# Kernel tuning notes

Hardware: AMD Instinct MI355X
Metric: run time of the kernel (lower is better)

The kernel has to match this reference:

```python
import jax, jax.numpy as jnp
import numpy as np

HID = 1024
HEADS = 16
HEAD_DIM = HID // HEADS
INTER = 4 * HID
EPS = 1e-6
SCALE = 1.0 / np.sqrt(HEAD_DIM)


def setup_inputs() -> dict:
    key = jax.random.key(0)
    ks = jax.random.split(key, 8)
    s = 0.02
    return {
        "x": jax.random.normal(ks[0], (2, 2048, HID), dtype=jnp.float32),
        "wq": jax.random.normal(ks[1], (HID, HID), dtype=jnp.float32) * s,
        "wk": jax.random.normal(ks[2], (HID, HID), dtype=jnp.float32) * s,
        "wv": jax.random.normal(ks[3], (HID, HID), dtype=jnp.float32) * s,
        "wo": jax.random.normal(ks[4], (HID, HID), dtype=jnp.float32) * s,
        "w_gate": jax.random.normal(ks[5], (INTER, HID), dtype=jnp.float32) * s,
        "w_up": jax.random.normal(ks[6], (INTER, HID), dtype=jnp.float32) * s,
        "w_down": jax.random.normal(ks[7], (HID, INTER), dtype=jnp.float32) * s,
        "norm1_w": jnp.ones((HID,), dtype=jnp.float32),
        "norm2_w": jnp.ones((HID,), dtype=jnp.float32),
    }


def _rmsnorm(x, w):
    rms = jnp.sqrt(jnp.mean(x * x, axis=-1, keepdims=True) + EPS)
    return x / rms * w


def reference(x, wq, wk, wv, wo, w_gate, w_up, w_down, norm1_w, norm2_w):
    b, s, _ = x.shape
    residual = x
    h = _rmsnorm(x, norm1_w)
    # projections: nn.Linear computes h @ W.T
    q = (h @ wq.T).reshape(b, s, HEADS, HEAD_DIM).transpose(0, 2, 1, 3)
    k = (h @ wk.T).reshape(b, s, HEADS, HEAD_DIM).transpose(0, 2, 1, 3)
    v = (h @ wv.T).reshape(b, s, HEADS, HEAD_DIM).transpose(0, 2, 1, 3)
    scores = jnp.einsum("bhqd,bhkd->bhqk", q, k) * SCALE
    attn = jax.nn.softmax(scores, axis=-1)
    out = jnp.einsum("bhqk,bhkd->bhqd", attn, v)
    out = out.transpose(0, 2, 1, 3).reshape(b, s, HID)
    x = residual + out @ wo.T
    residual = x
    h = _rmsnorm(x, norm2_w)
    gate = jax.nn.silu(h @ w_gate.T)
    up = h @ w_up.T
    mlp_out = (gate * up) @ w_down.T
    return residual + mlp_out
```

## Files before the change

### kernel.cpp

```cpp
#include <hip/hip_runtime.h>
#include <hip/hip_bf16.h>

#define HID 1024
#define SEQ 2048
#define NTOK 4096
#define ATT_SCALE 0.125f

typedef __attribute__((ext_vector_type(4))) float f32x4;
typedef __attribute__((ext_vector_type(16))) float f32x16;
typedef __attribute__((ext_vector_type(8))) __bf16 bf16x8;
typedef __attribute__((ext_vector_type(4))) __bf16 bf16x4;
typedef __bf16 bf16;

__device__ __forceinline__ bf16 f2bf(float f) { return (bf16)f; }

__device__ __forceinline__ void gld_lds16(const void* g, void* l) {
  __builtin_amdgcn_global_load_lds((const __attribute__((address_space(1))) void*)g,
                                   (__attribute__((address_space(3))) void*)l,
                                   16, 0, 0);
}

__device__ __forceinline__ f32x4 mfma16(bf16x8 a, bf16x8 b, f32x4 c) {
  return __builtin_amdgcn_mfma_f32_16x16x32_bf16(a, b, c, 0, 0, 0);
}
__device__ __forceinline__ f32x16 mfma32(bf16x8 a, bf16x8 b, f32x16 c) {
  return __builtin_amdgcn_mfma_f32_32x32x16_bf16(a, b, c, 0, 0, 0);
}

struct CvtArgs {
  const float* src[7];
  bf16* dst[7];
};

__global__ __launch_bounds__(256) void cvt_weights(CvtArgs a) {
  const int g = blockIdx.x * 256 + threadIdx.x;
  const int s = g >> 18;
  const int seg = s < 4 ? s : (s < 8 ? 4 : (s < 12 ? 5 : 6));
  const int start = seg < 4 ? (seg << 18) : (((seg - 4) << 20) + (1 << 20));
  const int loc = (g - start) << 2;
  const float4 v = *(const float4*)(a.src[seg] + loc);
  bf16x4 o = {f2bf(v.x), f2bf(v.y), f2bf(v.z), f2bf(v.w)};
  *(bf16x4*)(a.dst[seg] + loc) = o;
}

__global__ __launch_bounds__(256) void rmsnorm_k(const float* __restrict__ x,
                                                 const float* __restrict__ w,
                                                 bf16* __restrict__ h) {
  const int row = blockIdx.x;
  const int tid = threadIdx.x;
  const float4 xv = *(const float4*)(x + (size_t)row * HID + tid * 4);
  float ss = xv.x * xv.x + xv.y * xv.y + xv.z * xv.z + xv.w * xv.w;
#pragma unroll
  for (int m = 1; m < 64; m <<= 1) ss += __shfl_xor(ss, m, 64);
  __shared__ float wsum[4];
  if ((tid & 63) == 0) wsum[tid >> 6] = ss;
  __syncthreads();
  const float tot = wsum[0] + wsum[1] + wsum[2] + wsum[3];
  const float inv = rsqrtf(tot * (1.0f / HID) + 1e-6f);
  const float4 wv = *(const float4*)(w + tid * 4);
  bf16x4 o = {f2bf(xv.x * inv * wv.x), f2bf(xv.y * inv * wv.y),
              f2bf(xv.z * inv * wv.z), f2bf(xv.w * inv * wv.w)};
  *(bf16x4*)(h + (size_t)row * HID + tid * 4) = o;
}

__global__ __launch_bounds__(256) void rmsnorm_red_k(const float* __restrict__ x,
                                                     const float* __restrict__ p0,
                                                     const float* __restrict__ p1,
                                                     const float* __restrict__ w,
                                                     float* __restrict__ x2,
                                                     bf16* __restrict__ h) {
  const int row = blockIdx.x;
  const int tid = threadIdx.x;
  const size_t off = (size_t)row * HID + tid * 4;
  const float4 xa = *(const float4*)(x + off);
  const float4 pa = *(const float4*)(p0 + off);
  const float4 pb = *(const float4*)(p1 + off);
  float4 xv;
  xv.x = xa.x + pa.x + pb.x;
  xv.y = xa.y + pa.y + pb.y;
  xv.z = xa.z + pa.z + pb.z;
  xv.w = xa.w + pa.w + pb.w;
  *(float4*)(x2 + off) = xv;
  float ss = xv.x * xv.x + xv.y * xv.y + xv.z * xv.z + xv.w * xv.w;
#pragma unroll
  for (int m = 1; m < 64; m <<= 1) ss += __shfl_xor(ss, m, 64);
  __shared__ float wsum[4];
  if ((tid & 63) == 0) wsum[tid >> 6] = ss;
  __syncthreads();
  const float tot = wsum[0] + wsum[1] + wsum[2] + wsum[3];
  const float inv = rsqrtf(tot * (1.0f / HID) + 1e-6f);
  const float4 wv = *(const float4*)(w + tid * 4);
  bf16x4 o = {f2bf(xv.x * inv * wv.x), f2bf(xv.y * inv * wv.y),
              f2bf(xv.z * inv * wv.z), f2bf(xv.w * inv * wv.w)};
  *(bf16x4*)(h + off) = o;
}

__global__ __launch_bounds__(256) void add3_k(float* __restrict__ out,
                                              const float* __restrict__ p0,
                                              const float* __restrict__ p1) {
  const size_t i = ((size_t)blockIdx.x * 256 + threadIdx.x) * 4;
  const float4 a = *(const float4*)(out + i);
  const float4 b = *(const float4*)(p0 + i);
  const float4 c = *(const float4*)(p1 + i);
  float4 o;
  o.x = a.x + b.x + c.x;
  o.y = a.y + b.y + c.y;
  o.z = a.z + b.z + c.z;
  o.w = a.w + b.w + c.w;
  *(float4*)(out + i) = o;
}

__global__ __launch_bounds__(512, 2) void gemm256(const bf16* __restrict__ A,
                                                  const bf16* __restrict__ B,
                                                  bf16* __restrict__ C,
                                                  int N, int K) {
  alignas(16) __shared__ bf16 As[2][256][64];
  alignas(16) __shared__ bf16 Bs[2][256][64];
  const int tid = threadIdx.x;
  const int wid = tid >> 6, lane = tid & 63;
  const int wm = wid >> 2, wn = wid & 3;
  const int bm0 = blockIdx.y << 8, bn0 = blockIdx.x << 8;

  const int srow = (wid << 3) + (lane >> 3);
  const int gch = ((lane & 7) ^ (lane >> 3)) << 3;
  const bf16* gA = A + (size_t)(bm0 + srow) * K + gch;
  const bf16* gB = B + (size_t)(bn0 + srow) * K + gch;

  const int fr = lane & 15, fc = lane >> 4, fx = lane & 7;

  f32x4 acc[8][4] = {};
  const int nt = K >> 6;

  auto stage = [&](int c, int k0) {
#pragma unroll
    for (int i = 0; i < 4; ++i)
      gld_lds16(gA + (size_t)(i * 64) * K + k0, &As[c][i * 64 + (wid << 3)][0]);
#pragma unroll
    for (int i = 0; i < 4; ++i)
      gld_lds16(gB + (size_t)(i * 64) * K + k0, &Bs[c][i * 64 + (wid << 3)][0]);
  };

  stage(0, 0);
  stage(1, 64);
  asm volatile("s_waitcnt vmcnt(8)" ::: "memory");
  __builtin_amdgcn_s_barrier();
  __builtin_amdgcn_sched_barrier(0);

  for (int t = 0; t < nt; ++t) {
    const int c = t & 1;
    bf16x8 bfrag[2][4];
#pragma unroll
    for (int s = 0; s < 2; ++s)
#pragma unroll
      for (int n = 0; n < 4; ++n)
        bfrag[s][n] = *(const bf16x8*)&Bs[c][wn * 64 + n * 16 + fr]
                                         [(((s << 2) + fc) ^ fx) << 3];
#pragma unroll
    for (int q = 0; q < 4; ++q) {
      bf16x8 af[2][2];
#pragma unroll
      for (int mi = 0; mi < 2; ++mi)
#pragma unroll
        for (int s = 0; s < 2; ++s)
          af[mi][s] = *(const bf16x8*)&As[c][wm * 128 + (q * 2 + mi) * 16 + fr]
                                           [(((s << 2) + fc) ^ fx) << 3];
      __builtin_amdgcn_s_setprio(1);
#pragma unroll
      for (int mi = 0; mi < 2; ++mi)
#pragma unroll
        for (int n = 0; n < 4; ++n)
#pragma unroll
          for (int s = 0; s < 2; ++s)
            acc[q * 2 + mi][n] = mfma16(af[mi][s], bfrag[s][n], acc[q * 2 + mi][n]);
      __builtin_amdgcn_s_setprio(0);
    }
    __builtin_amdgcn_sched_barrier(0);
    __builtin_amdgcn_s_barrier();
    __builtin_amdgcn_sched_barrier(0);
    if (t + 2 < nt) {
      stage(c, (t + 2) << 6);
      asm volatile("s_waitcnt vmcnt(8)" ::: "memory");
    } else {
      asm volatile("s_waitcnt vmcnt(0)" ::: "memory");
    }
    __builtin_amdgcn_s_barrier();
    __builtin_amdgcn_sched_barrier(0);
  }

#pragma unroll
  for (int m = 0; m < 8; ++m) {
    const int row = bm0 + wm * 128 + m * 16 + (fc << 2);
#pragma unroll
    for (int n = 0; n < 4; ++n) {
      const int col = bn0 + wn * 64 + n * 16 + fr;
#pragma unroll
      for (int r = 0; r < 4; ++r)
        C[(size_t)(row + r) * N + col] = f2bf(acc[m][n][r]);
    }
  }
}

template <int EPI>
__global__ __launch_bounds__(256) void gemm_bt(const bf16* __restrict__ A, int lda,
                                               const bf16* __restrict__ B, int ldb,
                                               void* __restrict__ C,
                                               const float* __restrict__ R,
                                               int ldc, int K) {
  alignas(16) __shared__ bf16 As[128 * 32];
  alignas(16) __shared__ bf16 Bs[128 * 32];
  const int tid = threadIdx.x;
  const int wid = tid >> 6;
  const int lane = tid & 63;
  const int bm0 = blockIdx.y * 128;
  const int bn0 = blockIdx.x * 128;
  const int wr = wid >> 1, wc = wid & 1;
  const size_t koff = (size_t)blockIdx.z * K;

  f32x4 acc[4][4] = {};

  const int sr = tid >> 2;
  const int sc = (tid & 3) << 3;
  const bf16* gA = A + (size_t)(bm0 + sr) * lda + sc + koff;
  const bf16* gB = B + (size_t)(bn0 + sr) * ldb + sc + koff;
  bf16* lA = As + wid * 512;
  bf16* lB = Bs + wid * 512;
  const int frow = lane & 15;
  const int kofs = (lane >> 4) << 3;

  for (int k0 = 0; k0 < K; k0 += 32) {
    __syncthreads();
    gld_lds16(gA + k0, lA);
    gld_lds16(gA + k0 + (size_t)64 * lda, lA + 2048);
    gld_lds16(gB + k0, lB);
    gld_lds16(gB + k0 + (size_t)64 * ldb, lB + 2048);
    __syncthreads();
    bf16x8 af[4], bfr[4];
#pragma unroll
    for (int m = 0; m < 4; ++m)
      af[m] = *(const bf16x8*)(As + (wr * 64 + m * 16 + frow) * 32 + kofs);
#pragma unroll
    for (int n = 0; n < 4; ++n)
      bfr[n] = *(const bf16x8*)(Bs + (wc * 64 + n * 16 + frow) * 32 + kofs);
#pragma unroll
    for (int m = 0; m < 4; ++m)
#pragma unroll
      for (int n = 0; n < 4; ++n)
        acc[m][n] = mfma16(af[m], bfr[n], acc[m][n]);
  }

  float* P = (EPI == 2) ? (blockIdx.z ? (float*)R : (float*)C) : nullptr;
  const int er = bm0 + wr * 64 + ((lane >> 4) << 2);
  const int ec = bn0 + wc * 64 + (lane & 15);
#pragma unroll
  for (int m = 0; m < 4; ++m)
#pragma unroll
    for (int n = 0; n < 4; ++n)
#pragma unroll
      for (int r = 0; r < 4; ++r) {
        const size_t idx = (size_t)(er + m * 16 + r) * ldc + (ec + n * 16);
        if (EPI == 0)      ((bf16*)C)[idx] = f2bf(acc[m][n][r]);
        else if (EPI == 1) ((float*)C)[idx] = R[idx] + acc[m][n][r];
        else               P[idx] = acc[m][n][r];
      }
}

__global__ __launch_bounds__(256) void vtrans_k(const bf16* __restrict__ qkv,
                                                bf16* __restrict__ vt) {
  const int bh = blockIdx.y;
  const int b = bh >> 4, head = bh & 15;
  const int st0 = blockIdx.x * 64;
  const int wid = threadIdx.x >> 6, lane = threadIdx.x & 63;
  const bf16* src = qkv + ((size_t)b * SEQ + st0 + lane) * 3072 + 2 * HID + head * 64 + wid * 16;
  bf16* dst = vt + (size_t)bh * (64 * SEQ) + st0 + lane;
#pragma unroll
  for (int half = 0; half < 2; ++half) {
    bf16x8 v = *(const bf16x8*)(src + half * 8);
#pragma unroll
    for (int i = 0; i < 8; ++i)
      dst[(size_t)(wid * 16 + half * 8 + i) * SEQ] = v[i];
  }
}

__global__ __launch_bounds__(128) void attn_k(const bf16* __restrict__ qkv,
                                              const bf16* __restrict__ vt,
                                              bf16* __restrict__ attn_out) {
  const int bh = blockIdx.y;
  const int b = bh >> 4, head = bh & 15;
  const int tid = threadIdx.x, wid = tid >> 6, lane = tid & 63;
  const int l31 = lane & 31, h = lane >> 5;
  const int r7 = l31 & 7;

  alignas(16) __shared__ bf16 Ks[64 * 64];
  alignas(16) __shared__ bf16 Vs[64 * 64];

  const size_t tokq = (size_t)b * SEQ + blockIdx.x * 64 + wid * 32 + l31;
  bf16x8 qf[4];
#pragma unroll
  for (int s = 0; s < 4; ++s) {
    bf16x8 t = *(const bf16x8*)(qkv + tokq * 3072 + head * 64 + s * 16 + h * 8);
#pragma unroll
    for (int i = 0; i < 8; ++i) t[i] = f2bf((float)t[i] * ATT_SCALE);
    qf[s] = t;
  }

  const int sr = tid >> 1;
  const int sc = (tid & 1) * 32;
  const int p5 = sr & 31;
  const int keyr = (sr & 32) | (p5 & 16) | (((p5 >> 2) & 1) << 3) | (((p5 >> 3) & 1) << 2) | (p5 & 3);
  const bf16* kg = qkv + ((size_t)b * SEQ + keyr) * 3072 + HID + head * 64 + sc;
  const bf16* vg = vt + (size_t)bh * (64 * SEQ) + (size_t)sr * SEQ + sc;
  int wofs[4];
#pragma unroll
  for (int j = 0; j < 4; ++j)
    wofs[j] = sr * 64 + ((((sc >> 3) + j) ^ (sr & 7)) << 3);

  f32x16 o0 = {}, o1 = {};
  float m = -1e30f, l = 0.f;

  for (int t0 = 0; t0 < SEQ; t0 += 64) {
    __syncthreads();
#pragma unroll
    for (int j = 0; j < 4; ++j) {
      bf16x8 kv = *(const bf16x8*)(kg + (size_t)t0 * 3072 + j * 8);
      *(bf16x8*)(Ks + wofs[j]) = kv;
      bf16x8 vv = *(const bf16x8*)(vg + t0 + j * 8);
      *(bf16x8*)(Vs + wofs[j]) = vv;
    }
    __syncthreads();

    f32x16 s0 = {}, s1 = {};
#pragma unroll
    for (int s = 0; s < 4; ++s) {
      bf16x8 k0 = *(const bf16x8*)(Ks + l31 * 64 + (((2 * s + h) ^ r7) << 3));
      s0 = mfma32(k0, qf[s], s0);
      bf16x8 k1 = *(const bf16x8*)(Ks + (32 + l31) * 64 + (((2 * s + h) ^ r7) << 3));
      s1 = mfma32(k1, qf[s], s1);
    }

    float pmax = s0[0];
#pragma unroll
    for (int i = 1; i < 16; ++i) pmax = fmaxf(pmax, s0[i]);
#pragma unroll
    for (int i = 0; i < 16; ++i) pmax = fmaxf(pmax, s1[i]);
    pmax = fmaxf(pmax, __shfl_xor(pmax, 32, 64));
    const float mnew = fmaxf(m, pmax);
    const float al = __expf(m - mnew);
    m = mnew;

    bf16x8 pa[4];
    float sum = 0.f;
#pragma unroll
    for (int t = 0; t < 2; ++t)
#pragma unroll
      for (int j = 0; j < 8; ++j) {
        const float p = __expf(s0[8 * t + j] - mnew);
        sum += p;
        pa[t][j] = f2bf(p);
      }
#pragma unroll
    for (int t = 0; t < 2; ++t)
#pragma unroll
      for (int j = 0; j < 8; ++j) {
        const float p = __expf(s1[8 * t + j] - mnew);
        sum += p;
        pa[2 + t][j] = f2bf(p);
      }
    sum += __shfl_xor(sum, 32, 64);
    l = l * al + sum;
#pragma unroll
    for (int i = 0; i < 16; ++i) { o0[i] *= al; o1[i] *= al; }

#pragma unroll
    for (int t = 0; t < 4; ++t) {
      bf16x8 v0 = *(const bf16x8*)(Vs + l31 * 64 + (((2 * t + h) ^ r7) << 3));
      o0 = mfma32(v0, pa[t], o0);
      bf16x8 v1 = *(const bf16x8*)(Vs + (32 + l31) * 64 + (((2 * t + h) ^ r7) << 3));
      o1 = mfma32(v1, pa[t], o1);
    }
  }

  const float inv = 1.0f / l;
  bf16* obase = attn_out + tokq * HID + head * 64;
#pragma unroll
  for (int rq = 0; rq < 4; ++rq) {
    bf16x4 w0, w1;
#pragma unroll
    for (int i = 0; i < 4; ++i) {
      w0[i] = f2bf(o0[4 * rq + i] * inv);
      w1[i] = f2bf(o1[4 * rq + i] * inv);
    }
    *(bf16x4*)(obase + 8 * rq + 4 * h) = w0;
    *(bf16x4*)(obase + 32 + 8 * rq + 4 * h) = w1;
  }
}

__global__ __launch_bounds__(256) void silu_mul_k(bf16* __restrict__ gu) {
  const int t = blockIdx.x * 256 + threadIdx.x;
  const int row = t >> 9;
  const int j = (t & 511) << 3;
  bf16* p = gu + (size_t)row * 8192 + j;
  bf16x8 g8 = *(const bf16x8*)p;
  bf16x8 u8 = *(const bf16x8*)(p + 4096);
  bf16x8 o;
#pragma unroll
  for (int i = 0; i < 8; ++i) {
    const float g = (float)g8[i], u = (float)u8[i];
    const float s = g / (1.0f + __expf(-g));
    o[i] = f2bf(s * u);
  }
  *(bf16x8*)p = o;
}

extern "C" void kernel_launch(void* const* d_in, const int* in_sizes, int n_in,
                              void* d_out, int out_size, void* d_ws, size_t ws_size,
                              hipStream_t stream) {
  const float* x  = (const float*)d_in[0];
  const float* wq = (const float*)d_in[1];
  const float* wk = (const float*)d_in[2];
  const float* wv = (const float*)d_in[3];
  const float* wo = (const float*)d_in[4];
  const float* wg = (const float*)d_in[5];
  const float* wu = (const float*)d_in[6];
  const float* wd = (const float*)d_in[7];
  const float* n1 = (const float*)d_in[8];
  const float* n2 = (const float*)d_in[9];

  char* ws = (char*)d_ws;
  bf16* wqkv_b  = (bf16*)(ws);
  bf16* wo_b    = (bf16*)(ws + 6291456);
  bf16* wgu_b   = (bf16*)(ws + 8388608);
  bf16* wd_b    = (bf16*)(ws + 25165824);
  bf16* h       = (bf16*)(ws + 33554432);
  bf16* attnout = (bf16*)(ws + 41943040);
  bf16* qkv     = (bf16*)(ws + 50331648);
  bf16* vt      = (bf16*)(ws + 75497472);
  bf16* gu      = (bf16*)(ws + 50331648);
  float* x2     = (float*)d_out;

  float* pw0 = (float*)(ws + 50331648);
  float* pw1 = (float*)(ws + 67108864);
  float* pd0 = (float*)(ws);
  float* pd1 = (float*)(ws + 33554432);

  CvtArgs ca;
  ca.src[0] = wq; ca.dst[0] = wqkv_b;
  ca.src[1] = wk; ca.dst[1] = wqkv_b + 1048576;
  ca.src[2] = wv; ca.dst[2] = wqkv_b + 2097152;
  ca.src[3] = wo; ca.dst[3] = wo_b;
  ca.src[4] = wg; ca.dst[4] = wgu_b;
  ca.src[5] = wu; ca.dst[5] = wgu_b + 4194304;
  ca.src[6] = wd; ca.dst[6] = wd_b;

  cvt_weights<<<dim3(16384), dim3(256), 0, stream>>>(ca);
  rmsnorm_k<<<dim3(NTOK), dim3(256), 0, stream>>>(x, n1, h);
  gemm256<<<dim3(12, 16), dim3(512), 0, stream>>>(h, wqkv_b, qkv, 3072, 1024);
  vtrans_k<<<dim3(32, 32), dim3(256), 0, stream>>>(qkv, vt);
  attn_k<<<dim3(32, 32), dim3(128), 0, stream>>>(qkv, vt, attnout);
  gemm_bt<2><<<dim3(8, 32, 2), dim3(256), 0, stream>>>(attnout, 1024, wo_b, 1024,
                                                       (void*)pw0, (const float*)pw1, 1024, 512);
  rmsnorm_red_k<<<dim3(NTOK), dim3(256), 0, stream>>>(x, pw0, pw1, n2, x2, h);
  gemm256<<<dim3(32, 16), dim3(512), 0, stream>>>(h, wgu_b, gu, 8192, 1024);
  silu_mul_k<<<dim3(8192), dim3(256), 0, stream>>>(gu);
  gemm_bt<2><<<dim3(8, 32, 2), dim3(256), 0, stream>>>(gu, 8192, wd_b, 4096,
                                                       (void*)pd0, (const float*)pd1, 1024, 2048);
  add3_k<<<dim3(4096), dim3(256), 0, stream>>>(x2, pd0, pd1);
}
```

Measured before the change: 440.9 us.

## Double the attention block to 128 queries, prefetch K/V into registers, use lazy rescaling

The attention kernel now uses 4 waves per block covering 128 queries, so each K/V tile staged in shared memory is reused by twice as many queries. The next tile's K/V is loaded into registers while the current tile is computed. Softmax folds log2(e) into the Q scale and uses exp2f. Rescaling of the running max and accumulator is skipped unless some row's max grows by more than 8 (in log2 units). This cuts global loads and exp/rescale ALU work, at the cost of more registers, half as many blocks, and bounded growth of the unnormalized partial sums.

```diff
diff --git a/kernel.cpp b/kernel.cpp
--- a/kernel.cpp
+++ b/kernel.cpp
@@ -281,7 +281,7 @@
   }
 }
 
-__global__ __launch_bounds__(128) void attn_k(const bf16* __restrict__ qkv,
+__global__ __launch_bounds__(256) void attn_k(const bf16* __restrict__ qkv,
                                               const bf16* __restrict__ vt,
                                               bf16* __restrict__ attn_out) {
   const int bh = blockIdx.y;
@@ -293,40 +293,47 @@
   alignas(16) __shared__ bf16 Ks[64 * 64];
   alignas(16) __shared__ bf16 Vs[64 * 64];
 
-  const size_t tokq = (size_t)b * SEQ + blockIdx.x * 64 + wid * 32 + l31;
+  const float QSCALE = ATT_SCALE * 1.44269504088896f;
+  const size_t tokq = (size_t)b * SEQ + blockIdx.x * 128 + wid * 32 + l31;
   bf16x8 qf[4];
 #pragma unroll
   for (int s = 0; s < 4; ++s) {
     bf16x8 t = *(const bf16x8*)(qkv + tokq * 3072 + head * 64 + s * 16 + h * 8);
 #pragma unroll
-    for (int i = 0; i < 8; ++i) t[i] = f2bf((float)t[i] * ATT_SCALE);
+    for (int i = 0; i < 8; ++i) t[i] = f2bf((float)t[i] * QSCALE);
     qf[s] = t;
   }
 
-  const int sr = tid >> 1;
-  const int sc = (tid & 1) * 32;
+  const int sr = tid & 63;
+  const int c0 = tid >> 6;
   const int p5 = sr & 31;
   const int keyr = (sr & 32) | (p5 & 16) | (((p5 >> 2) & 1) << 3) | (((p5 >> 3) & 1) << 2) | (p5 & 3);
-  const bf16* kg = qkv + ((size_t)b * SEQ + keyr) * 3072 + HID + head * 64 + sc;
-  const bf16* vg = vt + (size_t)bh * (64 * SEQ) + (size_t)sr * SEQ + sc;
-  int wofs[4];
-#pragma unroll
-  for (int j = 0; j < 4; ++j)
-    wofs[j] = sr * 64 + ((((sc >> 3) + j) ^ (sr & 7)) << 3);
+  const bf16* kbase = qkv + ((size_t)b * SEQ + keyr) * 3072 + HID + head * 64 + c0 * 8;
+  const bf16* vbase = vt + (size_t)bh * (64 * SEQ) + (size_t)sr * SEQ + c0 * 8;
+  const int w0 = sr * 64 + ((c0 ^ (sr & 7)) << 3);
+  const int w1 = sr * 64 + (((c0 + 4) ^ (sr & 7)) << 3);
+
+  bf16x8 kr0 = *(const bf16x8*)(kbase);
+  bf16x8 kr1 = *(const bf16x8*)(kbase + 32);
+  bf16x8 vr0 = *(const bf16x8*)(vbase);
+  bf16x8 vr1 = *(const bf16x8*)(vbase + 32);
 
   f32x16 o0 = {}, o1 = {};
   float m = -1e30f, l = 0.f;
 
   for (int t0 = 0; t0 < SEQ; t0 += 64) {
     __syncthreads();
-#pragma unroll
-    for (int j = 0; j < 4; ++j) {
-      bf16x8 kv = *(const bf16x8*)(kg + (size_t)t0 * 3072 + j * 8);
-      *(bf16x8*)(Ks + wofs[j]) = kv;
-      bf16x8 vv = *(const bf16x8*)(vg + t0 + j * 8);
-      *(bf16x8*)(Vs + wofs[j]) = vv;
-    }
+    *(bf16x8*)(Ks + w0) = kr0;
+    *(bf16x8*)(Ks + w1) = kr1;
+    *(bf16x8*)(Vs + w0) = vr0;
+    *(bf16x8*)(Vs + w1) = vr1;
     __syncthreads();
+    if (t0 + 64 < SEQ) {
+      kr0 = *(const bf16x8*)(kbase + (size_t)(t0 + 64) * 3072);
+      kr1 = *(const bf16x8*)(kbase + (size_t)(t0 + 64) * 3072 + 32);
+      vr0 = *(const bf16x8*)(vbase + t0 + 64);
+      vr1 = *(const bf16x8*)(vbase + t0 + 96);
+    }
 
     f32x16 s0 = {}, s1 = {};
 #pragma unroll
@@ -343,9 +350,14 @@
 #pragma unroll
     for (int i = 0; i < 16; ++i) pmax = fmaxf(pmax, s1[i]);
     pmax = fmaxf(pmax, __shfl_xor(pmax, 32, 64));
-    const float mnew = fmaxf(m, pmax);
-    const float al = __expf(m - mnew);
-    m = mnew;
+    if (!__all(pmax <= m + 8.0f)) {
+      const float mnew = fmaxf(m, pmax);
+      const float al = exp2f(m - mnew);
+      l *= al;
+#pragma unroll
+      for (int i = 0; i < 16; ++i) { o0[i] *= al; o1[i] *= al; }
+      m = mnew;
+    }
 
     bf16x8 pa[4];
     float sum = 0.f;
@@ -353,7 +365,7 @@
     for (int t = 0; t < 2; ++t)
 #pragma unroll
       for (int j = 0; j < 8; ++j) {
-        const float p = __expf(s0[8 * t + j] - mnew);
+        const float p = exp2f(s0[8 * t + j] - m);
         sum += p;
         pa[t][j] = f2bf(p);
       }
@@ -361,14 +373,12 @@
     for (int t = 0; t < 2; ++t)
 #pragma unroll
       for (int j = 0; j < 8; ++j) {
-        const float p = __expf(s1[8 * t + j] - mnew);
+        const float p = exp2f(s1[8 * t + j] - m);
         sum += p;
         pa[2 + t][j] = f2bf(p);
       }
     sum += __shfl_xor(sum, 32, 64);
-    l = l * al + sum;
-#pragma unroll
-    for (int i = 0; i < 16; ++i) { o0[i] *= al; o1[i] *= al; }
+    l += sum;
 
 #pragma unroll
     for (int t = 0; t < 4; ++t) {
@@ -383,14 +393,14 @@
   bf16* obase = attn_out + tokq * HID + head * 64;
 #pragma unroll
   for (int rq = 0; rq < 4; ++rq) {
-    bf16x4 w0, w1;
+    bf16x4 w0v, w1v;
 #pragma unroll
     for (int i = 0; i < 4; ++i) {
-      w0[i] = f2bf(o0[4 * rq + i] * inv);
-      w1[i] = f2bf(o1[4 * rq + i] * inv);
-    }
-    *(bf16x4*)(obase + 8 * rq + 4 * h) = w0;
-    *(bf16x4*)(obase + 32 + 8 * rq + 4 * h) = w1;
+      w0v[i] = f2bf(o0[4 * rq + i] * inv);
+      w1v[i] = f2bf(o1[4 * rq + i] * inv);
+    }
+    *(bf16x4*)(obase + 8 * rq + 4 * h) = w0v;
+    *(bf16x4*)(obase + 32 + 8 * rq + 4 * h) = w1v;
   }
 }
 
@@ -455,7 +465,7 @@
   rmsnorm_k<<<dim3(NTOK), dim3(256), 0, stream>>>(x, n1, h);
   gemm256<<<dim3(12, 16), dim3(512), 0, stream>>>(h, wqkv_b, qkv, 3072, 1024);
   vtrans_k<<<dim3(32, 32), dim3(256), 0, stream>>>(qkv, vt);
-  attn_k<<<dim3(32, 32), dim3(128), 0, stream>>>(qkv, vt, attnout);
+  attn_k<<<dim3(16, 32), dim3(256), 0, stream>>>(qkv, vt, attnout);
   gemm_bt<2><<<dim3(8, 32, 2), dim3(256), 0, stream>>>(attnout, 1024, wo_b, 1024,
                                                        (void*)pw0, (const float*)pw1, 1024, 512);
   rmsnorm_red_k<<<dim3(NTOK), dim3(256), 0, stream>>>(x, pw0, pw1, n2, x2, h);
```

After: 441.0 us. About the same (+0.0%).
